# Performance work log

Measured on AMD Instinct MI355X. Metric: run time of the kernel, lower is better.

The kernel has to match this reference:

```python
import jax, jax.numpy as jnp
import numpy as np
import math

H, W = 180, 320          # frame_shape
RF = 16                  # rf_diameter
K = 20
T = 400                  # video frames
FRAME_RATE = 120.0
ALPHA, BETA, GAMMA = 50.0, 1.0, 0.0   # soft-rectifier params
CENTER_SIGMA, SURROUND_SIGMA = 4.0, 8.0
CENTER_STR, SURROUND_STR = 1.0, -0.8
COVERAGE = 0.5


def _mosaic():
    # hexagonal lattice of cell centers (replicates _tile_cells)
    s = CENTER_SIGMA / COVERAGE
    B = np.array([[s, s / 2.0], [0.0, s * math.sqrt(3.0) / 2.0]], dtype=np.float64)
    Binv = np.linalg.inv(B)
    margin = CENTER_SIGMA / 2.0
    corners = np.array([[0, 0], [W, 0], [0, H], [W, H]], dtype=np.float64)
    lc = corners @ Binv.T
    n0, n1 = int(np.floor(lc[:, 0].min())) - 1, int(np.ceil(lc[:, 0].max())) + 1
    m0, m1 = int(np.floor(lc[:, 1].min())) - 1, int(np.ceil(lc[:, 1].max())) + 1
    pos = []
    for m in range(m0, m1 + 1):
        for n in range(n0, n1 + 1):
            p = np.array([float(n), float(m)]) @ B.T
            if margin <= p[0] <= W - margin and margin <= p[1] <= H - margin:
                pos.append((p[0], p[1]))
    return np.array(pos, dtype=np.float32)


def _rf_indices(mosaic):
    # flat pixel indices into the (H+2RF, W+2RF) zero-padded frame
    pw = W + 2 * RF
    yy, xx = np.meshgrid(np.arange(RF), np.arange(RF), indexing='ij')
    local = (yy * pw + xx).ravel()
    out = []
    for x0, y0 in mosaic:
        v = math.floor(y0 - RF / 2.0) + RF
        h = math.floor(x0 - RF / 2.0) + RF
        out.append(local + v * pw + h)
    return np.stack(out).astype(np.int32)


def _filter():
    # DoG spatial filter
    c = RF / 2.0
    yy, xx = np.meshgrid(np.arange(RF, dtype=np.float32), np.arange(RF, dtype=np.float32), indexing='ij')
    d2 = (xx - c) ** 2 + (yy - c) ** 2
    cen = np.exp(-d2 / (2 * CENTER_SIGMA ** 2)); cen /= cen.sum()
    sur = np.exp(-d2 / (2 * SURROUND_SIGMA ** 2)); sur /= sur.sum()
    spatial = CENTER_STR * cen + SURROUND_STR * sur
    # biphasic temporal filter with smooth onset, ON cell, flipped
    dt = 1000.0 / FRAME_RATE
    t = np.arange(K, dtype=np.float32) * dt
    l1 = 1.0 * np.exp(-(t - 40.0) ** 2 / (2 * 20.0 ** 2))
    l2 = 0.6 * np.exp(-(t - 100.0) ** 2 / (2 * 40.0 ** 2))
    onset = 1.0 - np.exp(-t / 15.0)
    temporal = ((l1 - l2) * onset)[::-1].copy()
    st = temporal[:, None, None] * spatial[None]
    st = st / np.linalg.norm(st)
    return st.reshape(-1).astype(np.float32)


def setup_inputs() -> dict:
    key = jax.random.key(0)
    x = jax.random.normal(key, (T, H, W), dtype=jnp.float32)
    mosaic = _mosaic()
    return {
        'x': x,
        'w': jnp.asarray(_filter()),                    # (K*RF*RF,)
        'rf_indices': jnp.asarray(_rf_indices(mosaic)),  # (N_cells, RF*RF)
    }


def reference(x, w, rf_indices):
    # x: (T,H,W); w: (K*RF*RF,); rf_indices: (N, RF*RF) int32
    xp = jnp.pad(x, ((0, 0), (RF, RF), (RF, RF)))
    flat = xp.reshape(x.shape[0], -1)              # (T, (H+2RF)*(W+2RF))
    patches = jnp.take(flat, rf_indices, axis=1)   # (T, N, RF*RF) irregular gather
    wk = w.reshape(K, RF * RF)
    # spatial projection against each temporal tap
    y = jnp.einsum('tnp,kp->tnk', patches, wk)     # (T, N, K)
    n_win = x.shape[0] - K + 1
    # generator[i, n] = sum_k y[i+k, n, k]  (sliding-window spatiotemporal dot)
    g = y[0:n_win, :, 0]
    for k in range(1, K):
        g = g + y[k:k + n_win, :, k]
    out = ALPHA * jax.nn.softplus(BETA * (g - GAMMA))  # soft-rectifier nonlinearity
    return out.T                                    # (N_cells, n_windows)
```

## Files before the change

kernel.cpp:

```cpp
#include <hip/hip_runtime.h>
#include <math.h>

constexpr int H_ = 180, W_ = 320, RF_ = 16, K_ = 20, T_ = 400;
constexpr int HW_ = H_ * W_;
constexpr int NWIN = T_ - K_ + 1;
constexpr int PW   = W_ + 2 * RF_;
constexpr float ALPHA = 50.0f, BETA = 1.0f, GAMMA = 0.0f;
constexpr int NXCD = 8;
constexpr int T_PER_XCD = T_ / NXCD;
constexpr int T_HALF = T_PER_XCD / 2;
constexpr int CH = 8;

template <int CTRL>
__device__ inline float dpp_add(float v) {
    int s = __builtin_amdgcn_update_dpp(0, __float_as_int(v), CTRL, 0xF, 0xF, true);
    return v + __int_as_float(s);
}
__device__ inline float swz_xor4_add(float v) {
    return v + __int_as_float(
        __builtin_amdgcn_ds_swizzle(__float_as_int(v), 0x101F));
}
#if __has_builtin(__builtin_amdgcn_permlane32_swap)
__device__ inline float pl32_merge(float a, float b) {
    auto r = __builtin_amdgcn_permlane32_swap(
        __float_as_uint(a), __float_as_uint(b), false, false);
    return __uint_as_float(r[0]) + __uint_as_float(r[1]);
}
#else
__device__ inline float pl32_merge(float a, float b) {
    bool hi = (threadIdx.x & 32) != 0;
    float keep = hi ? b : a, send = hi ? a : b;
    return keep + __shfl_xor(send, 32, 64);
}
#endif
#if __has_builtin(__builtin_amdgcn_permlane16_swap)
__device__ inline float pl16_merge(float a, float b) {
    auto r = __builtin_amdgcn_permlane16_swap(
        __float_as_uint(a), __float_as_uint(b), false, false);
    return __uint_as_float(r[0]) + __uint_as_float(r[1]);
}
#else
__device__ inline float pl16_merge(float a, float b) {
    bool hi = (threadIdx.x & 16) != 0;
    float keep = hi ? b : a, send = hi ? a : b;
    return keep + __shfl_xor(send, 16, 64);
}
#endif
__device__ inline float allred64(float v) {
    v = dpp_add<0xB1>(v);
    v = dpp_add<0x4E>(v);
    v = swz_xor4_add(v);
    v = dpp_add<0x128>(v);
    v = pl16_merge(v, v);
    v = pl32_merge(v, v);
    return v;
}

__device__ inline float multired8(const float* acc, bool b8) {
    float m0 = pl32_merge(acc[0], acc[4]);
    float m1 = pl32_merge(acc[1], acc[5]);
    float m2 = pl32_merge(acc[2], acc[6]);
    float m3 = pl32_merge(acc[3], acc[7]);
    float n0 = pl16_merge(m0, m2);
    float n1 = pl16_merge(m1, m3);
    float c0v = dpp_add<0x128>(n0);
    float c1v = dpp_add<0x128>(n1);
    float C = b8 ? c1v : c0v;
    C = dpp_add<0xB1>(C);
    C = dpp_add<0x4E>(C);
    C = swz_xor4_add(C);
    return C;
}

__global__ __launch_bounds__(1024) void prep_kernel(
    const float* __restrict__ w, const int* __restrict__ rf,
    float* __restrict__ spatial, float* __restrict__ temporal,
    int* __restrict__ cnt, int4* __restrict__ tasks, int N)
{
    __shared__ float ss[32];
    int tid = threadIdx.x, wv = tid >> 6, l = tid & 63;
    if (tid == 0) *cnt = 0;
    __syncthreads();

    if (wv < 8) {
        for (int k = wv; k < K_; k += 8) {
            float s = 0.0f;
#pragma unroll
            for (int j = 0; j < 4; ++j) {
                float v = w[k * 256 + l + j * 64];
                s = fmaf(v, v, s);
            }
            s = allred64(s);
            if (l == 0) ss[k] = s;
        }
    } else {
        for (int i = tid - 512; 2 * i < N; i += 512) {
            int n1 = 2 * i, n2 = 2 * i + 1;
            int b1 = rf[n1 * 256];
            int v1 = b1 / PW;
            int pn2 = n1, b2 = b1, v2 = v1;
            bool paired = false;
            if (n2 < N) {
                b2 = rf[n2 * 256];
                v2 = b2 / PW;
                paired = (v2 == v1);
            }
            {
                int r0  = v1 - RF_;
                int c01 = (b1 - v1 * PW) - RF_;
                int r0c = min(max(r0, 0), H_ - RF_);
                int c0c1 = min(max(c01, 0), W_ - RF_);
                int c02  = paired ? ((b2 - v2 * PW) - RF_) : c01;
                int c0c2 = min(max(c02, 0), W_ - RF_);
                pn2 = paired ? n2 : n1;
                int4 d;
                d.x = n1 | (pn2 << 16);
                d.y = r0c * W_ + c0c1;
                d.z = c0c2 - c0c1;
                d.w = (r0c - r0 + 8) | ((c0c1 - c01 + 8) << 8)
                                     | ((c0c2 - c02 + 8) << 16);
                tasks[atomicAdd(cnt, 1)] = d;
            }
            if (!paired && n2 < N) {
                int r0  = v2 - RF_;
                int c02 = (b2 - v2 * PW) - RF_;
                int r0c = min(max(r0, 0), H_ - RF_);
                int c0c2 = min(max(c02, 0), W_ - RF_);
                int4 d;
                d.x = n2 | (n2 << 16);
                d.y = r0c * W_ + c0c2;
                d.z = 0;
                d.w = (r0c - r0 + 8) | ((c0c2 - c02 + 8) << 8)
                                     | ((c0c2 - c02 + 8) << 16);
                tasks[atomicAdd(cnt, 1)] = d;
            }
        }
    }
    __syncthreads();

    float best = -1.0f;
    int k0 = 0;
    for (int k = 0; k < K_; ++k) {
        float v = ss[k];
        if (v > best) { best = v; k0 = k; }
    }
    if (wv < 8) {
        for (int k = wv; k < K_; k += 8) {
            float d = 0.0f;
#pragma unroll
            for (int j = 0; j < 4; ++j)
                d = fmaf(w[k * 256 + l + j * 64], w[k0 * 256 + l + j * 64], d);
            d = allred64(d);
            if (l == 0) temporal[k] = d / best;
        }
    }
    if (tid < 256) spatial[tid] = w[k0 * 256 + tid];
}

__global__ __launch_bounds__(256) void stage1_kernel(
    const float* __restrict__ x, const int4* __restrict__ tasks,
    const int* __restrict__ cnt, const float* __restrict__ spatial,
    float* __restrict__ y)
{
    int lane = threadIdx.x & 63;
    int wid  = threadIdx.x >> 6;

    int b    = blockIdx.x;
    int xcd  = b & (NXCD - 1);
    int rest = b >> 3;
    int half = rest & 1;
    int tg   = rest >> 1;

    int taskid = tg * 4 + wid;
    if (taskid >= *cnt) return;

    int4 d = tasks[taskid];
    int n1 = d.x & 0xFFFF;
    int n2 = d.x >> 16;
    int delta = d.z;
    int dr  = (d.w & 0xFF) - 8;
    int dc1 = ((d.w >> 8) & 0xFF) - 8;
    int dc2 = ((d.w >> 16) & 0xFF) - 8;

    int t0 = xcd * T_PER_XCD + half * T_HALF;

    int r = lane >> 2;
    int s = lane & 3;

    int rr = r + dr;
    bool rok = (rr >= 0) & (rr < RF_);
    int cc1 = 4 * s + dc1;
    int cc2 = 4 * s + dc2;
    float4 w1 = make_float4(0.f, 0.f, 0.f, 0.f), w2 = w1;
    if (rok & (cc1 >= 0) & (cc1 < RF_))
        w1 = *reinterpret_cast<const float4*>(spatial + rr * RF_ + cc1);
    if (rok & (cc2 >= 0) & (cc2 < RF_))
        w2 = *reinterpret_cast<const float4*>(spatial + rr * RF_ + cc2);

    int offA = d.y + r * W_ + 4 * s;
    const float* xp = x + (size_t)t0 * HW_;
    float* yp1 = y + (size_t)n1 * T_ + t0;
    float* yp2 = y + (size_t)n2 * T_ + t0;

    bool b8 = (lane & 8) != 0;

    for (int tt = 0; tt < 24; tt += CH) {
        float4 A[CH], B[CH];
#pragma unroll
        for (int j = 0; j < CH; ++j) {
            const float* fp = xp + (size_t)(tt + j) * HW_ + offA;
            A[j] = *reinterpret_cast<const float4*>(fp);
            B[j] = *reinterpret_cast<const float4*>(fp + delta);
        }
        float a1[CH], a2[CH];
#pragma unroll
        for (int j = 0; j < CH; ++j) {
            float u = A[j].x * w1.x;
            u = fmaf(A[j].y, w1.y, u);
            u = fmaf(A[j].z, w1.z, u);
            a1[j] = fmaf(A[j].w, w1.w, u);
            float v = B[j].x * w2.x;
            v = fmaf(B[j].y, w2.y, v);
            v = fmaf(B[j].z, w2.z, v);
            a2[j] = fmaf(B[j].w, w2.w, v);
        }
        float C1 = multired8(a1, b8);
        float C2 = multired8(a2, b8);
        if ((lane & 7) == 0) {
            yp1[tt + (lane >> 3)] = C1;
            yp2[tt + (lane >> 3)] = C2;
        }
    }

    {
        const float* fp = xp + (size_t)24 * HW_ + offA;
        float4 A = *reinterpret_cast<const float4*>(fp);
        float4 B = *reinterpret_cast<const float4*>(fp + delta);
        float u = A.x * w1.x;
        u = fmaf(A.y, w1.y, u);
        u = fmaf(A.z, w1.z, u);
        u = fmaf(A.w, w1.w, u);
        float v = B.x * w2.x;
        v = fmaf(B.y, w2.y, v);
        v = fmaf(B.z, w2.z, v);
        v = fmaf(B.w, w2.w, v);
        u = allred64(u);
        v = allred64(v);
        if (lane == 0) {
            yp1[24] = u;
            yp2[24] = v;
        }
    }
}

__global__ void stage2_kernel(const float* __restrict__ y,
                              const float* __restrict__ temporal,
                              float* __restrict__ out, int N)
{
    __shared__ float tw[K_];
    if (threadIdx.x < K_) tw[threadIdx.x] = temporal[threadIdx.x];
    __syncthreads();

    int n  = blockIdx.x;
    int t0 = threadIdx.x;
    if (n >= N || t0 >= NWIN) return;

    const float* yn = y + (size_t)n * T_;
    float g = 0.0f;
#pragma unroll
    for (int k = 0; k < K_; ++k)
        g = fmaf(yn[t0 + k], tw[k], g);

    float z = BETA * (g - GAMMA);
    float sp = fmaxf(z, 0.0f) + log1pf(expf(-fabsf(z)));
    out[n * NWIN + t0] = ALPHA * sp;
}

extern "C" void kernel_launch(void* const* d_in, const int* in_sizes, int n_in,
                              void* d_out, int out_size, void* d_ws, size_t ws_size,
                              hipStream_t stream)
{
    const float* x  = (const float*)d_in[0];
    const float* w  = (const float*)d_in[1];
    const int*   rf = (const int*)d_in[2];

    int N = in_sizes[2] / (RF_ * RF_);

    float* spatial  = (float*)d_ws;
    float* temporal = spatial + 256;
    int*   cnt      = (int*)d_ws + 320;
    int4*  tasks    = (int4*)((int*)d_ws + 384);
    float* y        = (float*)d_ws + 384 + 4 * N;

    int NTG = (N + 3) / 4;
    prep_kernel<<<1, 1024, 0, stream>>>(w, rf, spatial, temporal, cnt, tasks, N);
    stage1_kernel<<<NXCD * NTG * 2, 256, 0, stream>>>(x, tasks, cnt, spatial, y);
    stage2_kernel<<<N, 384, 0, stream>>>(y, temporal, (float*)d_out, N);
}
```

Measured before the change: 40.93 us.

## Bucket stage-1 tasks by patch row and split frames into time slices

```diff
diff --git a/kernel.cpp b/kernel.cpp
--- a/kernel.cpp
+++ b/kernel.cpp
@@ -6,10 +6,9 @@
 constexpr int NWIN = T_ - K_ + 1;
 constexpr int PW   = W_ + 2 * RF_;
 constexpr float ALPHA = 50.0f, BETA = 1.0f, GAMMA = 0.0f;
-constexpr int NXCD = 8;
-constexpr int T_PER_XCD = T_ / NXCD;
-constexpr int T_HALF = T_PER_XCD / 2;
-constexpr int CH = 8;
+constexpr int NROWS = 165;
+constexpr int CAP   = 32;
+constexpr int NSLICE = 32;
 
 template <int CTRL>
 __device__ inline float dpp_add(float v) {
@@ -55,7 +54,6 @@
     v = pl32_merge(v, v);
     return v;
 }
-
 __device__ inline float multired8(const float* acc, bool b8) {
     float m0 = pl32_merge(acc[0], acc[4]);
     float m1 = pl32_merge(acc[1], acc[5]);
@@ -79,7 +77,7 @@
 {
     __shared__ float ss[32];
     int tid = threadIdx.x, wv = tid >> 6, l = tid & 63;
-    if (tid == 0) *cnt = 0;
+    if (tid < 256) cnt[tid] = 0;
     __syncthreads();
 
     if (wv < 8) {
@@ -94,45 +92,36 @@
             if (l == 0) ss[k] = s;
         }
     } else {
+        auto emit = [&](int n1, int n2, int b1, int b2) {
+            int v1  = b1 / PW;
+            int r0  = v1 - RF_;
+            int c01 = (b1 - v1 * PW) - RF_;
+            int r0c = min(max(r0, 0), H_ - RF_);
+            int c0c1 = min(max(c01, 0), W_ - RF_);
+            int c02  = (b2 - (b2 / PW) * PW) - RF_;
+            int c0c2 = min(max(c02, 0), W_ - RF_);
+            int slot = atomicAdd(&cnt[r0c], 1);
+            int4 d;
+            d.x = n1 | (n2 << 16);
+            d.y = r0c * W_ + c0c1;
+            d.z = c0c2 - c0c1;
+            d.w = (r0c - r0 + 8) | ((c0c1 - c01 + 8) << 8)
+                                 | ((c0c2 - c02 + 8) << 16);
+            tasks[r0c * CAP + slot] = d;
+        };
         for (int i = tid - 512; 2 * i < N; i += 512) {
             int n1 = 2 * i, n2 = 2 * i + 1;
             int b1 = rf[n1 * 256];
-            int v1 = b1 / PW;
-            int pn2 = n1, b2 = b1, v2 = v1;
-            bool paired = false;
             if (n2 < N) {
-                b2 = rf[n2 * 256];
-                v2 = b2 / PW;
-                paired = (v2 == v1);
-            }
-            {
-                int r0  = v1 - RF_;
-                int c01 = (b1 - v1 * PW) - RF_;
-                int r0c = min(max(r0, 0), H_ - RF_);
-                int c0c1 = min(max(c01, 0), W_ - RF_);
-                int c02  = paired ? ((b2 - v2 * PW) - RF_) : c01;
-                int c0c2 = min(max(c02, 0), W_ - RF_);
-                pn2 = paired ? n2 : n1;
-                int4 d;
-                d.x = n1 | (pn2 << 16);
-                d.y = r0c * W_ + c0c1;
-                d.z = c0c2 - c0c1;
-                d.w = (r0c - r0 + 8) | ((c0c1 - c01 + 8) << 8)
-                                     | ((c0c2 - c02 + 8) << 16);
-                tasks[atomicAdd(cnt, 1)] = d;
-            }
-            if (!paired && n2 < N) {
-                int r0  = v2 - RF_;
-                int c02 = (b2 - v2 * PW) - RF_;
-                int r0c = min(max(r0, 0), H_ - RF_);
-                int c0c2 = min(max(c02, 0), W_ - RF_);
-                int4 d;
-                d.x = n2 | (n2 << 16);
-                d.y = r0c * W_ + c0c2;
-                d.z = 0;
-                d.w = (r0c - r0 + 8) | ((c0c2 - c02 + 8) << 8)
-                                     | ((c0c2 - c02 + 8) << 16);
-                tasks[atomicAdd(cnt, 1)] = d;
+                int b2 = rf[n2 * 256];
+                if (b2 / PW == b1 / PW) {
+                    emit(n1, n2, b1, b2);
+                } else {
+                    emit(n1, n1, b1, b1);
+                    emit(n2, n2, b2, b2);
+                }
+            } else {
+                emit(n1, n1, b1, b1);
             }
         }
     }
@@ -158,98 +147,68 @@
 }
 
 __global__ __launch_bounds__(256) void stage1_kernel(
-    const float* __restrict__ x, const int4* __restrict__ tasks,
-    const int* __restrict__ cnt, const float* __restrict__ spatial,
+    const float* __restrict__ x, const int* __restrict__ cnt,
+    const int4* __restrict__ tasks, const float* __restrict__ spatial,
     float* __restrict__ y)
 {
+    int bi  = blockIdx.x;
+    int slo = bi & 7;
+    int shi = (bi >> 3) & 3;
+    int row = bi >> 5;
+    int s   = (shi << 3) | slo;
+    int t0   = (s < 16) ? s * 13 : 208 + (s - 16) * 12;
+    int tlen = (s < 16) ? 13 : 12;
+
+    int count = cnt[row];
+    if (count == 0) return;
+
     int lane = threadIdx.x & 63;
     int wid  = threadIdx.x >> 6;
-
-    int b    = blockIdx.x;
-    int xcd  = b & (NXCD - 1);
-    int rest = b >> 3;
-    int half = rest & 1;
-    int tg   = rest >> 1;
-
-    int taskid = tg * 4 + wid;
-    if (taskid >= *cnt) return;
-
-    int4 d = tasks[taskid];
-    int n1 = d.x & 0xFFFF;
-    int n2 = d.x >> 16;
-    int delta = d.z;
-    int dr  = (d.w & 0xFF) - 8;
-    int dc1 = ((d.w >> 8) & 0xFF) - 8;
-    int dc2 = ((d.w >> 16) & 0xFF) - 8;
-
-    int t0 = xcd * T_PER_XCD + half * T_HALF;
-
     int r = lane >> 2;
-    int s = lane & 3;
-
-    int rr = r + dr;
-    bool rok = (rr >= 0) & (rr < RF_);
-    int cc1 = 4 * s + dc1;
-    int cc2 = 4 * s + dc2;
-    float4 w1 = make_float4(0.f, 0.f, 0.f, 0.f), w2 = w1;
-    if (rok & (cc1 >= 0) & (cc1 < RF_))
-        w1 = *reinterpret_cast<const float4*>(spatial + rr * RF_ + cc1);
-    if (rok & (cc2 >= 0) & (cc2 < RF_))
-        w2 = *reinterpret_cast<const float4*>(spatial + rr * RF_ + cc2);
-
-    int offA = d.y + r * W_ + 4 * s;
-    const float* xp = x + (size_t)t0 * HW_;
-    float* yp1 = y + (size_t)n1 * T_ + t0;
-    float* yp2 = y + (size_t)n2 * T_ + t0;
-
+    int q = lane & 3;
     bool b8 = (lane & 8) != 0;
-
-    for (int tt = 0; tt < 24; tt += CH) {
-        float4 A[CH], B[CH];
-#pragma unroll
-        for (int j = 0; j < CH; ++j) {
-            const float* fp = xp + (size_t)(tt + j) * HW_ + offA;
-            A[j] = *reinterpret_cast<const float4*>(fp);
-            B[j] = *reinterpret_cast<const float4*>(fp + delta);
-        }
-        float a1[CH], a2[CH];
-#pragma unroll
-        for (int j = 0; j < CH; ++j) {
-            float u = A[j].x * w1.x;
-            u = fmaf(A[j].y, w1.y, u);
-            u = fmaf(A[j].z, w1.z, u);
-            a1[j] = fmaf(A[j].w, w1.w, u);
-            float v = B[j].x * w2.x;
-            v = fmaf(B[j].y, w2.y, v);
-            v = fmaf(B[j].z, w2.z, v);
-            a2[j] = fmaf(B[j].w, w2.w, v);
-        }
-        float C1 = multired8(a1, b8);
-        float C2 = multired8(a2, b8);
-        if ((lane & 7) == 0) {
-            yp1[tt + (lane >> 3)] = C1;
-            yp2[tt + (lane >> 3)] = C2;
-        }
-    }
-
-    {
-        const float* fp = xp + (size_t)24 * HW_ + offA;
-        float4 A = *reinterpret_cast<const float4*>(fp);
-        float4 B = *reinterpret_cast<const float4*>(fp + delta);
-        float u = A.x * w1.x;
-        u = fmaf(A.y, w1.y, u);
-        u = fmaf(A.z, w1.z, u);
-        u = fmaf(A.w, w1.w, u);
-        float v = B.x * w2.x;
-        v = fmaf(B.y, w2.y, v);
-        v = fmaf(B.z, w2.z, v);
-        v = fmaf(B.w, w2.w, v);
-        u = allred64(u);
-        v = allred64(v);
-        if (lane == 0) {
-            yp1[24] = u;
-            yp2[24] = v;
-        }
+    const int4* list = tasks + row * CAP;
+
+    for (int f = 0; f < tlen; ++f) {
+        int t = t0 + f;
+        const float* fp = x + (size_t)t * HW_;
+        for (int ti = wid; ti < count; ti += 4) {
+            int4 d = list[ti];
+            int n1 = d.x & 0xFFFF;
+            int n2 = (d.x >> 16) & 0xFFFF;
+            int dr  = (d.w & 0xFF) - 8;
+            int dc1 = ((d.w >> 8) & 0xFF) - 8;
+            int dc2 = ((d.w >> 16) & 0xFF) - 8;
+
+            int rr = r + dr;
+            bool rok = (rr >= 0) & (rr < RF_);
+            int cc1 = 4 * q + dc1;
+            int cc2 = 4 * q + dc2;
+            float4 w1 = make_float4(0.f, 0.f, 0.f, 0.f), w2 = w1;
+            if (rok & (cc1 >= 0) & (cc1 < RF_))
+                w1 = *reinterpret_cast<const float4*>(spatial + rr * RF_ + cc1);
+            if (rok & (cc2 >= 0) & (cc2 < RF_))
+                w2 = *reinterpret_cast<const float4*>(spatial + rr * RF_ + cc2);
+
+            int off = d.y + r * W_ + 4 * q;
+            float4 A = *reinterpret_cast<const float4*>(fp + off);
+            float4 B = *reinterpret_cast<const float4*>(fp + off + d.z);
+
+            float u = A.x * w1.x;
+            u = fmaf(A.y, w1.y, u);
+            u = fmaf(A.z, w1.z, u);
+            u = fmaf(A.w, w1.w, u);
+            float v = B.x * w2.x;
+            v = fmaf(B.y, w2.y, v);
+            v = fmaf(B.z, w2.z, v);
+            v = fmaf(B.w, w2.w, v);
+
+            float acc[8] = {u, v, 0.f, 0.f, 0.f, 0.f, 0.f, 0.f};
+            float C = multired8(acc, b8);
+            if (lane == 0)      y[(size_t)n1 * T_ + t] = C;
+            else if (lane == 8) y[(size_t)n2 * T_ + t] = C;
+        }
+        __syncthreads();
     }
 }
 
@@ -289,11 +248,10 @@
     float* spatial  = (float*)d_ws;
     float* temporal = spatial + 256;
     int*   cnt      = (int*)d_ws + 320;
-    int4*  tasks    = (int4*)((int*)d_ws + 384);
-    float* y        = (float*)d_ws + 384 + 4 * N;
-
-    int NTG = (N + 3) / 4;
+    int4*  tasks    = (int4*)((int*)d_ws + 576);
+    float* y        = (float*)d_ws + 576 + 4 * NROWS * CAP;
+
     prep_kernel<<<1, 1024, 0, stream>>>(w, rf, spatial, temporal, cnt, tasks, N);
-    stage1_kernel<<<NXCD * NTG * 2, 256, 0, stream>>>(x, tasks, cnt, spatial, y);
+    stage1_kernel<<<NROWS * NSLICE, 256, 0, stream>>>(x, cnt, tasks, spatial, y);
     stage2_kernel<<<N, 384, 0, stream>>>(y, temporal, (float*)d_out, N);
 }
```

Result: slower. 91.47 us (+123.5%).
